# Optimization experiments

Measured on AMD Instinct MI355X. Metric: run time of the kernel, lower is better.

The kernel has to match this reference:

```python
import jax, jax.numpy as jnp
import numpy as np

# --- static config (from init_kwargs) ---
DT, TAU_M = 1.0, 10.0
BETA = float(np.exp(-DT / TAU_M))
THRESH = 1.0
SLOPE = 25.0  # fast_sigmoid surrogate slope
T, B, DEPTH, SZ = 50, 16, 1, 64
C1, C2, K1, K2 = 16, 16, 5, 5
S1 = SZ - K1 + 1   # 60
S2 = S1 - K2 + 1   # 56
NCONV2 = C2 * S2 * S2  # 50176
NREC = 256

@jax.custom_vjp
def spike(m):
    return (m > THRESH).astype(m.dtype)

def _spk_fwd(m):
    return spike(m), m

def _spk_bwd(m, g):
    # fast_sigmoid surrogate: d spk / d mem = 1 / (slope*|mem - thr| + 1)^2
    return (g / (SLOPE * jnp.abs(m - THRESH) + 1.0) ** 2,)

spike.defvjp(_spk_fwd, _spk_bwd)

def lif(inp, mem, zero_reset=False):
    # snntorch Leaky: reset computed from previous mem, detached
    reset = jax.lax.stop_gradient((mem > THRESH).astype(mem.dtype))
    base = BETA * mem + inp
    mem_new = base * (1.0 - reset) if zero_reset else base - reset * THRESH
    return spike(mem_new), mem_new

def conv(x, w, b):
    y = jax.lax.conv_general_dilated(x, w, (1, 1), 'VALID',
                                     dimension_numbers=('NCHW', 'OIHW', 'NCHW'))
    return y + b[None, :, None, None]

def deconv(x, w, b):
    # torch ConvTranspose2d (stride 1, no pad), weight [Cin, Cout, kh, kw]
    k = w.shape[-1]
    wf = jnp.flip(w, (2, 3)).transpose(1, 0, 2, 3)  # -> OIHW, O=Cout
    y = jax.lax.conv_general_dilated(x, wf, (1, 1),
                                     [(k - 1, k - 1), (k - 1, k - 1)],
                                     dimension_numbers=('NCHW', 'OIHW', 'NCHW'))
    return y + b[None, :, None, None]

def setup_inputs() -> dict:
    key = jax.random.key(0)
    ks = jax.random.split(key, 16)
    def w(k, shape, fan_in):
        return (jax.random.normal(k, shape, jnp.float32) / np.sqrt(fan_in)).astype(jnp.float32)
    # osc_of_t per process_params: R_m*I_osc/v_th*(1-beta)*(-1+cos(omega*t - pi))/2
    tarr = np.arange(0, T * DT, DT)
    omega = 2 * np.pi * 0.01
    osc = (1.0 * 1.0 / 1.0) * (1 - BETA) * (-1 + np.cos(omega * tarr - np.pi)) / 2
    return {
        'x': jax.random.normal(ks[0], (T, B, DEPTH, SZ, SZ), jnp.float32),
        'osc': jnp.asarray(osc, jnp.float32),
        'conv1_w': w(ks[1], (C1, DEPTH, K1, K1), DEPTH * K1 * K1),
        'conv1_b': jnp.zeros((C1,), jnp.float32),
        'conv2_w': w(ks[2], (C2, C1, K2, K2), C1 * K2 * K2),
        'conv2_b': jnp.zeros((C2,), jnp.float32),
        'ff_in_w': w(ks[3], (NREC, NCONV2), NCONV2),
        'ff_in_b': jnp.zeros((NREC,), jnp.float32),
        'ff_rec_w': w(ks[4], (NREC, NREC), NREC),
        'ff_rec_b': jnp.zeros((NREC,), jnp.float32),
        'ff_out_w': w(ks[5], (NCONV2, NREC), NREC),
        'ff_out_b': jnp.zeros((NCONV2,), jnp.float32),
        'deconv2_w': w(ks[6], (C2, C1, K2, K2), C2 * K2 * K2),
        'deconv2_b': jnp.zeros((C1,), jnp.float32),
        'recon_w': w(ks[7], (C1, DEPTH, K1, K1), C1 * K1 * K1),
        'recon_b': jnp.zeros((DEPTH,), jnp.float32),
    }

def reference(x, osc, conv1_w, conv1_b, conv2_w, conv2_b,
              ff_in_w, ff_in_b, ff_rec_w, ff_rec_b, ff_out_w, ff_out_b,
              deconv2_w, deconv2_b, recon_w, recon_b):
    mem_c1 = jnp.zeros((B, C1, S1, S1), x.dtype)
    mem_c2 = jnp.zeros((B, C2, S2, S2), x.dtype)
    mem_rec = jnp.zeros((B, NREC), x.dtype)
    mem_d2 = jnp.zeros((B, C1, S1, S1), x.dtype)
    mem_rc = jnp.zeros((B, DEPTH, SZ, SZ), x.dtype)
    spk_rec0 = jnp.zeros((B, NREC), x.dtype)

    def step(carry, xt_osc):
        mem_c1, mem_c2, mem_rec, mem_d2, mem_rc, spk_rec = carry
        xt, o = xt_osc
        spk1, mem_c1 = lif(conv(xt, conv1_w, conv1_b) + o, mem_c1)
        spk2, mem_c2 = lif(conv(spk1, conv2_w, conv2_b) + o, mem_c2)
        curr_in = spk2.reshape(B, -1) @ ff_in_w.T + ff_in_b
        curr_rec = spk_rec @ ff_rec_w.T + ff_rec_b
        spk_rec, mem_rec = lif(curr_in + curr_rec + o, mem_rec, zero_reset=True)
        curr_out = (spk_rec @ ff_out_w.T + ff_out_b).reshape(B, C2, S2, S2)
        spk_d2, mem_d2 = lif(deconv(curr_out, deconv2_w, deconv2_b) + o, mem_d2)
        spk_rc, mem_rc = lif(deconv(spk_d2, recon_w, recon_b) + o, mem_rc)
        return (mem_c1, mem_c2, mem_rec, mem_d2, mem_rc, spk_rec), (spk_rec, spk_rc)

    carry0 = (mem_c1, mem_c2, mem_rec, mem_d2, mem_rc, spk_rec0)
    _, (spk_recs, spk_outs) = jax.lax.scan(step, carry0, (x, osc))
    return spk_recs, spk_outs
```

## Files before the change

kernel.cpp:

```cpp
#include <hip/hip_runtime.h>

#define BETA_F 0.9048374180359595f

constexpr int B_ = 16, C1_ = 16, C2_ = 16;
constexpr int S1 = 60, S2 = 56;
constexpr int NCONV2 = C2_ * S2 * S2;
constexpr int NREC = 256;

__device__ float g_mem_c1x[2 * 921600];
__device__ float g_mem_c2[802816];
__device__ float g_mem_rec[4096];
__device__ float g_mem_d2[921600];
__device__ float g_mem_rc[65536];
__device__ unsigned char g_spk2bx[2][B_ * NCONV2];
__device__ float g_currx[2][B_ * NCONV2];
__device__ float g_spkd2x[2][921600];
__device__ float g_spkrec2[2 * 4096];
__device__ float g_woutT[NREC * NCONV2];

__device__ __forceinline__ float lif_sub(float mp, float inp, float& mn_out) {
    float rst = mp > 1.f ? 1.f : 0.f;
    float base = __fadd_rn(__fmul_rn(BETA_F, mp), inp);
    float mn = __fsub_rn(base, rst);
    mn_out = mn;
    return mn > 1.f ? 1.f : 0.f;
}

__global__ void k_transpose(const float* __restrict__ Wout) {
    __shared__ float T[64][65];
    int m0 = blockIdx.x * 64;
    for (int k0 = 0; k0 < 256; k0 += 64) {
        __syncthreads();
        for (int e = threadIdx.x; e < 64 * 64; e += 256) {
            int i = e >> 6, k = e & 63;
            T[i][k] = Wout[(size_t)(m0 + i) * 256 + k0 + k];
        }
        __syncthreads();
        for (int e = threadIdx.x; e < 64 * 64; e += 256) {
            int k = e >> 6, i = e & 63;
            g_woutT[(size_t)(k0 + k) * NCONV2 + m0 + i] = T[i][k];
        }
    }
}

__global__ __launch_bounds__(256)
void k_wave(int kw,
            const float* __restrict__ x, const float* __restrict__ osc,
            const float* __restrict__ w1, const float* __restrict__ b1,
            const float* __restrict__ w2, const float* __restrict__ b2,
            const float* __restrict__ win, const float* __restrict__ bin,
            const float* __restrict__ wrec, const float* __restrict__ brec,
            const float* __restrict__ bout,
            const float* __restrict__ wd2, const float* __restrict__ bd2,
            const float* __restrict__ wrc, const float* __restrict__ brc,
            float* __restrict__ out_recs, float* __restrict__ out_outs) {
    __shared__ float smem[8704];
    const int r = blockIdx.x;
    const int tid = threadIdx.x;

    if (r < 448) {
        int t = kw;
        if (t > 49) return;
        int first = (t == 0) ? 1 : 0;
        float* xw = smem;
        float* s1 = smem + 768;
        int tile = r % 14, b = (r / 14) & 15, half = r / 224;
        int y0 = 4 * tile;
        int y1 = (tile == 13) ? 60 : (y0 + 4);
        const float* xin = x + ((size_t)t * B_ + b) * 4096;
        for (int e = tid; e < 12 * 64; e += 256)
            xw[e] = xin[(y0 + (e >> 6)) * 64 + (e & 63)];
        __syncthreads();

        int par = t & 1;
        float* mc1_new = g_mem_c1x + (size_t)par * 921600;
        const float* mc1_old = g_mem_c1x + (size_t)(1 - par) * 921600;
        unsigned char* spk2b = g_spk2bx[par];
        float osct = osc[t];
#pragma unroll 1
        for (int c = 0; c < 16; c++) {
            const float* wc = w1 + c * 25;
            float bc = b1[c];
            for (int e = tid; e < 8 * 60; e += 256) {
                int rr = e / 60, col = e % 60;
                float s = 0.f;
#pragma unroll
                for (int ky = 0; ky < 5; ky++)
#pragma unroll
                    for (int kx = 0; kx < 5; kx++)
                        s = fmaf(xw[(rr + ky) * 64 + col + kx], wc[ky * 5 + kx], s);
                float inp = __fadd_rn(__fadd_rn(s, bc), osct);
                int gr = y0 + rr;
                int gidx = ((b * 16 + c) * 60 + gr) * 60 + col;
                float mp = first ? 0.f : mc1_old[gidx];
                float mn;
                float spk = lif_sub(mp, inp, mn);
                if (half == 0 && gr >= y0 && gr < y1) mc1_new[gidx] = mn;
                s1[c * 480 + e] = spk;
            }
        }
        __syncthreads();

        if (tid >= 224) return;
        int p = tile * 224 + tid;
        int yy = p / 56, xx = p % 56;
        int c2lo = half * 8;
        float acc[8];
#pragma unroll
        for (int u = 0; u < 8; u++) acc[u] = 0.f;
#pragma unroll 1
        for (int ci = 0; ci < 16; ci++) {
            const float* ip = s1 + ci * 480 + (yy - y0) * 60 + xx;
            float ipv[25];
#pragma unroll
            for (int ky = 0; ky < 5; ky++)
#pragma unroll
                for (int kx = 0; kx < 5; kx++)
                    ipv[ky * 5 + kx] = ip[ky * 60 + kx];
#pragma unroll
            for (int u = 0; u < 8; u++) {
                const float* wp = w2 + (c2lo + u) * 400 + ci * 25;
                float s = acc[u];
#pragma unroll
                for (int k = 0; k < 25; k++)
                    s = fmaf(ipv[k], wp[k], s);
                acc[u] = s;
            }
        }
#pragma unroll 1
        for (int u = 0; u < 8; u++) {
            int c2 = c2lo + u;
            float inp = __fadd_rn(__fadd_rn(acc[u], b2[c2]), osct);
            int idx = (b * 16 + c2) * 3136 + p;
            float mp = first ? 0.f : g_mem_c2[idx];
            float mn;
            float spk = lif_sub(mp, inp, mn);
            g_mem_c2[idx] = mn;
            spk2b[idx] = (unsigned char)(spk > 0.5f ? 1 : 0);
        }
    } else if (r < 1472) {
        int t = kw - 1;
        if (t < 0 || t > 49) return;
        int first = (t == 0) ? 1 : 0;
        float* red = smem;
        float* sprev = smem + 256;
        float* cur = smem + 1280;
        int bid = r - 448;
        int n = ((bid >> 5) << 3) + (bid & 7);
        int bg = ((bid >> 3) & 3) * 4;
        int par = t & 1;
        const float* sp_old = g_spkrec2 + (size_t)(1 - par) * 4096;
#pragma unroll
        for (int l = 0; l < 4; l++) {
            int e = tid + l * 256;
            sprev[e] = first ? 0.f : sp_old[(bg + (e >> 8)) * 256 + (e & 255)];
        }
        const unsigned char* sbase = g_spk2bx[par];
        const float* wrow = win + (size_t)n * NCONV2;
        const unsigned char* s0 = sbase + (size_t)(bg + 0) * NCONV2;
        const unsigned char* s1p = sbase + (size_t)(bg + 1) * NCONV2;
        const unsigned char* s2 = sbase + (size_t)(bg + 2) * NCONV2;
        const unsigned char* s3 = sbase + (size_t)(bg + 3) * NCONV2;
        float a0 = 0.f, a1 = 0.f, a2 = 0.f, a3 = 0.f;
        for (int j = 0; j < 49; j++) {
            int k = tid + j * 1024;
            float w0 = wrow[k];
            float wA = wrow[k + 256];
            float wB = wrow[k + 512];
            float wC = wrow[k + 768];
            unsigned char p00 = s0[k],       p01 = s1p[k],       p02 = s2[k],       p03 = s3[k];
            unsigned char p10 = s0[k + 256], p11 = s1p[k + 256], p12 = s2[k + 256], p13 = s3[k + 256];
            unsigned char p20 = s0[k + 512], p21 = s1p[k + 512], p22 = s2[k + 512], p23 = s3[k + 512];
            unsigned char p30 = s0[k + 768], p31 = s1p[k + 768], p32 = s2[k + 768], p33 = s3[k + 768];
            a0 = fmaf((float)p00, w0, a0); a1 = fmaf((float)p01, w0, a1);
            a2 = fmaf((float)p02, w0, a2); a3 = fmaf((float)p03, w0, a3);
            a0 = fmaf((float)p10, wA, a0); a1 = fmaf((float)p11, wA, a1);
            a2 = fmaf((float)p12, wA, a2); a3 = fmaf((float)p13, wA, a3);
            a0 = fmaf((float)p20, wB, a0); a1 = fmaf((float)p21, wB, a1);
            a2 = fmaf((float)p22, wB, a2); a3 = fmaf((float)p23, wB, a3);
            a0 = fmaf((float)p30, wC, a0); a1 = fmaf((float)p31, wC, a1);
            a2 = fmaf((float)p32, wC, a2); a3 = fmaf((float)p33, wC, a3);
        }
        float accs[4] = {a0, a1, a2, a3};
#pragma unroll
        for (int u = 0; u < 4; u++) {
            red[tid] = accs[u];
            __syncthreads();
            for (int st = 128; st > 0; st >>= 1) {
                if (tid < st) red[tid] = __fadd_rn(red[tid], red[tid + st]);
                __syncthreads();
            }
            if (tid == 0) cur[u] = red[0];
            __syncthreads();
        }
        if (tid < 4) {
            int bb = bg + tid;
            const float* wr = wrec + (size_t)n * 256;
            float acc = 0.f;
            for (int k = 0; k < 256; k++) acc = fmaf(sprev[tid * 256 + k], wr[k], acc);
            float cin = __fadd_rn(cur[tid], bin[n]);
            float crc = __fadd_rn(acc, brec[n]);
            float inp = __fadd_rn(__fadd_rn(cin, crc), osc[t]);
            int idx = bb * 256 + n;
            float mp = first ? 0.f : g_mem_rec[idx];
            float rst = mp > 1.f ? 1.f : 0.f;
            float base = __fadd_rn(__fmul_rn(BETA_F, mp), inp);
            float mn = (rst > 0.f) ? 0.f : base;
            g_mem_rec[idx] = mn;
            float spk = mn > 1.f ? 1.f : 0.f;
            g_spkrec2[(size_t)par * 4096 + idx] = spk;
            out_recs[(size_t)t * 4096 + idx] = spk;
        }
    } else if (r < 1864) {
        int t = kw - 2;
        if (t < 0 || t > 49) return;
        float* S = smem;
        int r2 = r - 1472;
        int mblk = r2 % 196;
        int bhalf = (r2 / 196) * 8;
        int par = t & 1;
#pragma unroll
        for (int l = 0; l < 8; l++) {
            int e = tid + l * 256;
            S[(e >> 8) * 256 + (e & 255)] =
                g_spkrec2[(size_t)par * 4096 + (bhalf + (e >> 8)) * 256 + (e & 255)];
        }
        __syncthreads();
        int m = mblk * 256 + tid;
        float* currw = g_currx[par];
        float acc[8];
#pragma unroll
        for (int b = 0; b < 8; b++) acc[b] = 0.f;
        for (int k = 0; k < 256; k++) {
            float w = g_woutT[(size_t)k * NCONV2 + m];
#pragma unroll
            for (int b = 0; b < 8; b++) acc[b] = fmaf(S[b * 256 + k], w, acc[b]);
        }
        float bb = bout[m];
#pragma unroll
        for (int b = 0; b < 8; b++)
            currw[(size_t)(bhalf + b) * NCONV2 + m] = __fadd_rn(acc[b], bb);
    } else if (r < 2344) {
        int t = kw - 3;
        if (t < 0 || t > 49) return;
        int first = (t == 0) ? 1 : 0;
        float* sd = smem;
        int r3 = r - 1864;
        int tile = r3 % 15, b = (r3 / 15) & 15, half = r3 / 240;
        int r0 = 4 * tile;
        int y0p = r0 - 4;
        int par = t & 1;
        const float* in = g_currx[par] + (size_t)b * NCONV2;
        for (int e = tid; e < 16 * 8 * 64; e += 256) {
            int ci = e / 512;
            int rem = e - ci * 512;
            int rr = rem >> 6, j = rem & 63;
            int iy = y0p + rr;
            int ix = j - 4;
            float v = (iy >= 0 && iy < 56 && ix >= 0 && ix < 56)
                        ? in[ci * 3136 + iy * 56 + ix] : 0.f;
            sd[e] = v;
        }
        __syncthreads();
        if (tid >= 240) return;
        int p = r0 * 60 + tid;
        int yy = p / 60, xx = p % 60;
        int colo = half * 8;
        float acc[8];
#pragma unroll
        for (int u = 0; u < 8; u++) acc[u] = 0.f;
#pragma unroll
        for (int kp = 0; kp < 5; kp++) {
            int rr = yy - r0 + kp;
#pragma unroll 1
            for (int ci = 0; ci < 16; ci++) {
                const float* ip = sd + ci * 512 + rr * 64 + xx;
                float ipv[5];
#pragma unroll
                for (int kq = 0; kq < 5; kq++) ipv[kq] = ip[kq];
#pragma unroll
                for (int u = 0; u < 8; u++) {
                    const float* wp = wd2 + (ci * 16 + colo + u) * 25 + (4 - kp) * 5;
                    float s = acc[u];
#pragma unroll
                    for (int kq = 0; kq < 5; kq++)
                        s = fmaf(ipv[kq], wp[4 - kq], s);
                    acc[u] = s;
                }
            }
        }
        float osct = osc[t];
        float* spkd2w = g_spkd2x[par];
#pragma unroll 1
        for (int u = 0; u < 8; u++) {
            int co = colo + u;
            float inp = __fadd_rn(__fadd_rn(acc[u], bd2[co]), osct);
            int idx = (b * 16 + co) * 3600 + p;
            float mp = first ? 0.f : g_mem_d2[idx];
            float mn;
            float spk = lif_sub(mp, inp, mn);
            g_mem_d2[idx] = mn;
            spkd2w[idx] = spk;
        }
    } else {
        int t = kw - 4;
        if (t < 0 || t > 49) return;
        int first = (t == 0) ? 1 : 0;
        float* sd = smem;
        int r4 = r - 2344;
        int tile = r4 & 15, b = r4 >> 4;
        int yymin = tile * 4;
        int y0p = yymin - 4;
        int par = t & 1;
        const float* in = g_spkd2x[par] + (size_t)b * 16 * 3600;
        for (int e = tid; e < 16 * 8 * 68; e += 256) {
            int ci = e / 544;
            int rem = e - ci * 544;
            int rr = rem / 68, j = rem - rr * 68;
            int iy = y0p + rr;
            int ix = j - 4;
            float v = (iy >= 0 && iy < 60 && ix >= 0 && ix < 60)
                        ? in[ci * 3600 + iy * 60 + ix] : 0.f;
            sd[e] = v;
        }
        __syncthreads();
        int p = tile * 256 + tid;
        int yy = p >> 6, xx = p & 63;
        float s = 0.f;
#pragma unroll
        for (int kp = 0; kp < 5; kp++) {
            int rr = yy - yymin + kp;
#pragma unroll 1
            for (int ci = 0; ci < 16; ci++) {
                const float* ip = sd + ci * 544 + rr * 68 + xx;
                const float* wp = wrc + ci * 25 + (4 - kp) * 5;
#pragma unroll
                for (int kq = 0; kq < 5; kq++)
                    s = fmaf(ip[kq], wp[4 - kq], s);
            }
        }
        float inp = __fadd_rn(__fadd_rn(s, brc[0]), osc[t]);
        int idx = b * 4096 + p;
        float mp = first ? 0.f : g_mem_rc[idx];
        float mn;
        float spk = lif_sub(mp, inp, mn);
        g_mem_rc[idx] = mn;
        out_outs[(size_t)t * B_ * 4096 + idx] = spk;
    }
}

extern "C" void kernel_launch(void* const* d_in, const int* in_sizes, int n_in,
                              void* d_out, int out_size, void* d_ws, size_t ws_size,
                              hipStream_t stream) {
    const float* x    = (const float*)d_in[0];
    const float* osc  = (const float*)d_in[1];
    const float* w1   = (const float*)d_in[2];
    const float* b1   = (const float*)d_in[3];
    const float* w2   = (const float*)d_in[4];
    const float* b2   = (const float*)d_in[5];
    const float* win  = (const float*)d_in[6];
    const float* bin  = (const float*)d_in[7];
    const float* wrec = (const float*)d_in[8];
    const float* brec = (const float*)d_in[9];
    const float* wout = (const float*)d_in[10];
    const float* bout = (const float*)d_in[11];
    const float* wd2  = (const float*)d_in[12];
    const float* bd2  = (const float*)d_in[13];
    const float* wrc  = (const float*)d_in[14];
    const float* brc  = (const float*)d_in[15];

    float* out = (float*)d_out;
    float* out_recs = out;
    float* out_outs = out + 50 * 16 * 256;

    k_transpose<<<784, 256, 0, stream>>>(wout);
    for (int kw = 0; kw < 54; kw++) {
        k_wave<<<2600, 256, 0, stream>>>(kw, x, osc, w1, b1, w2, b2, win, bin,
                                         wrec, brec, bout, wd2, bd2, wrc, brc,
                                         out_recs, out_outs);
    }
}
```

Baseline: 5.531 ms.

## Interleave conv2 spikes by batch, unroll ff_in loop, split recon tiles finer

Stores conv2 spike bytes batch-interleaved (16 batches per position) so the ff_in stage loads four batches with one uchar4 load instead of four scattered byte loads, and unrolls that loop twice. Conv1 now reads the input directly from global memory instead of staging it in shared memory, which drops one barrier. The recon stage is split into twice as many smaller tiles using 128 threads each, and the grid grows to match; the ff_out loop gets unroll 4. The interleaved layout makes conv2's byte stores strided, and half the threads in each recon block sit idle.

```diff
diff --git a/kernel.cpp b/kernel.cpp
--- a/kernel.cpp
+++ b/kernel.cpp
@@ -12,7 +12,7 @@
 __device__ float g_mem_rec[4096];
 __device__ float g_mem_d2[921600];
 __device__ float g_mem_rc[65536];
-__device__ unsigned char g_spk2bx[2][B_ * NCONV2];
+__device__ unsigned char g_spkpx[2][NCONV2 * 16];
 __device__ float g_currx[2][B_ * NCONV2];
 __device__ float g_spkd2x[2][921600];
 __device__ float g_spkrec2[2 * 4096];
@@ -54,7 +54,7 @@
             const float* __restrict__ wd2, const float* __restrict__ bd2,
             const float* __restrict__ wrc, const float* __restrict__ brc,
             float* __restrict__ out_recs, float* __restrict__ out_outs) {
-    __shared__ float smem[8704];
+    __shared__ float smem[8192];
     const int r = blockIdx.x;
     const int tid = threadIdx.x;
 
@@ -62,20 +62,16 @@
         int t = kw;
         if (t > 49) return;
         int first = (t == 0) ? 1 : 0;
-        float* xw = smem;
-        float* s1 = smem + 768;
+        float* s1 = smem;
         int tile = r % 14, b = (r / 14) & 15, half = r / 224;
         int y0 = 4 * tile;
         int y1 = (tile == 13) ? 60 : (y0 + 4);
         const float* xin = x + ((size_t)t * B_ + b) * 4096;
-        for (int e = tid; e < 12 * 64; e += 256)
-            xw[e] = xin[(y0 + (e >> 6)) * 64 + (e & 63)];
-        __syncthreads();
 
         int par = t & 1;
         float* mc1_new = g_mem_c1x + (size_t)par * 921600;
         const float* mc1_old = g_mem_c1x + (size_t)(1 - par) * 921600;
-        unsigned char* spk2b = g_spk2bx[par];
+        unsigned char* spkp = g_spkpx[par];
         float osct = osc[t];
 #pragma unroll 1
         for (int c = 0; c < 16; c++) {
@@ -88,14 +84,14 @@
                 for (int ky = 0; ky < 5; ky++)
 #pragma unroll
                     for (int kx = 0; kx < 5; kx++)
-                        s = fmaf(xw[(rr + ky) * 64 + col + kx], wc[ky * 5 + kx], s);
+                        s = fmaf(xin[(y0 + rr + ky) * 64 + col + kx], wc[ky * 5 + kx], s);
                 float inp = __fadd_rn(__fadd_rn(s, bc), osct);
                 int gr = y0 + rr;
                 int gidx = ((b * 16 + c) * 60 + gr) * 60 + col;
                 float mp = first ? 0.f : mc1_old[gidx];
                 float mn;
                 float spk = lif_sub(mp, inp, mn);
-                if (half == 0 && gr >= y0 && gr < y1) mc1_new[gidx] = mn;
+                if (half == 0 && gr < y1) mc1_new[gidx] = mn;
                 s1[c * 480 + e] = spk;
             }
         }
@@ -136,7 +132,7 @@
             float mn;
             float spk = lif_sub(mp, inp, mn);
             g_mem_c2[idx] = mn;
-            spk2b[idx] = (unsigned char)(spk > 0.5f ? 1 : 0);
+            spkp[(size_t)(c2 * 3136 + p) * 16 + b] = (unsigned char)(spk > 0.5f ? 1 : 0);
         }
     } else if (r < 1472) {
         int t = kw - 1;
@@ -155,31 +151,64 @@
             int e = tid + l * 256;
             sprev[e] = first ? 0.f : sp_old[(bg + (e >> 8)) * 256 + (e & 255)];
         }
-        const unsigned char* sbase = g_spk2bx[par];
+        const unsigned char* spb = g_spkpx[par] + bg;
         const float* wrow = win + (size_t)n * NCONV2;
-        const unsigned char* s0 = sbase + (size_t)(bg + 0) * NCONV2;
-        const unsigned char* s1p = sbase + (size_t)(bg + 1) * NCONV2;
-        const unsigned char* s2 = sbase + (size_t)(bg + 2) * NCONV2;
-        const unsigned char* s3 = sbase + (size_t)(bg + 3) * NCONV2;
         float a0 = 0.f, a1 = 0.f, a2 = 0.f, a3 = 0.f;
-        for (int j = 0; j < 49; j++) {
-            int k = tid + j * 1024;
+#pragma unroll 1
+        for (int jj = 0; jj < 24; jj++) {
+            int k = tid + (2 * jj) * 1024;
+            int k2 = k + 1024;
             float w0 = wrow[k];
             float wA = wrow[k + 256];
             float wB = wrow[k + 512];
             float wC = wrow[k + 768];
-            unsigned char p00 = s0[k],       p01 = s1p[k],       p02 = s2[k],       p03 = s3[k];
-            unsigned char p10 = s0[k + 256], p11 = s1p[k + 256], p12 = s2[k + 256], p13 = s3[k + 256];
-            unsigned char p20 = s0[k + 512], p21 = s1p[k + 512], p22 = s2[k + 512], p23 = s3[k + 512];
-            unsigned char p30 = s0[k + 768], p31 = s1p[k + 768], p32 = s2[k + 768], p33 = s3[k + 768];
-            a0 = fmaf((float)p00, w0, a0); a1 = fmaf((float)p01, w0, a1);
-            a2 = fmaf((float)p02, w0, a2); a3 = fmaf((float)p03, w0, a3);
-            a0 = fmaf((float)p10, wA, a0); a1 = fmaf((float)p11, wA, a1);
-            a2 = fmaf((float)p12, wA, a2); a3 = fmaf((float)p13, wA, a3);
-            a0 = fmaf((float)p20, wB, a0); a1 = fmaf((float)p21, wB, a1);
-            a2 = fmaf((float)p22, wB, a2); a3 = fmaf((float)p23, wB, a3);
-            a0 = fmaf((float)p30, wC, a0); a1 = fmaf((float)p31, wC, a1);
-            a2 = fmaf((float)p32, wC, a2); a3 = fmaf((float)p33, wC, a3);
+            float v0 = wrow[k2];
+            float vA = wrow[k2 + 256];
+            float vB = wrow[k2 + 512];
+            float vC = wrow[k2 + 768];
+            uchar4 q0 = *reinterpret_cast<const uchar4*>(spb + (size_t)k * 16);
+            uchar4 q1 = *reinterpret_cast<const uchar4*>(spb + (size_t)(k + 256) * 16);
+            uchar4 q2 = *reinterpret_cast<const uchar4*>(spb + (size_t)(k + 512) * 16);
+            uchar4 q3 = *reinterpret_cast<const uchar4*>(spb + (size_t)(k + 768) * 16);
+            uchar4 r0 = *reinterpret_cast<const uchar4*>(spb + (size_t)k2 * 16);
+            uchar4 r1 = *reinterpret_cast<const uchar4*>(spb + (size_t)(k2 + 256) * 16);
+            uchar4 r2 = *reinterpret_cast<const uchar4*>(spb + (size_t)(k2 + 512) * 16);
+            uchar4 r3 = *reinterpret_cast<const uchar4*>(spb + (size_t)(k2 + 768) * 16);
+            a0 = fmaf((float)q0.x, w0, a0); a1 = fmaf((float)q0.y, w0, a1);
+            a2 = fmaf((float)q0.z, w0, a2); a3 = fmaf((float)q0.w, w0, a3);
+            a0 = fmaf((float)q1.x, wA, a0); a1 = fmaf((float)q1.y, wA, a1);
+            a2 = fmaf((float)q1.z, wA, a2); a3 = fmaf((float)q1.w, wA, a3);
+            a0 = fmaf((float)q2.x, wB, a0); a1 = fmaf((float)q2.y, wB, a1);
+            a2 = fmaf((float)q2.z, wB, a2); a3 = fmaf((float)q2.w, wB, a3);
+            a0 = fmaf((float)q3.x, wC, a0); a1 = fmaf((float)q3.y, wC, a1);
+            a2 = fmaf((float)q3.z, wC, a2); a3 = fmaf((float)q3.w, wC, a3);
+            a0 = fmaf((float)r0.x, v0, a0); a1 = fmaf((float)r0.y, v0, a1);
+            a2 = fmaf((float)r0.z, v0, a2); a3 = fmaf((float)r0.w, v0, a3);
+            a0 = fmaf((float)r1.x, vA, a0); a1 = fmaf((float)r1.y, vA, a1);
+            a2 = fmaf((float)r1.z, vA, a2); a3 = fmaf((float)r1.w, vA, a3);
+            a0 = fmaf((float)r2.x, vB, a0); a1 = fmaf((float)r2.y, vB, a1);
+            a2 = fmaf((float)r2.z, vB, a2); a3 = fmaf((float)r2.w, vB, a3);
+            a0 = fmaf((float)r3.x, vC, a0); a1 = fmaf((float)r3.y, vC, a1);
+            a2 = fmaf((float)r3.z, vC, a2); a3 = fmaf((float)r3.w, vC, a3);
+        }
+        {
+            int k = tid + 48 * 1024;
+            float w0 = wrow[k];
+            float wA = wrow[k + 256];
+            float wB = wrow[k + 512];
+            float wC = wrow[k + 768];
+            uchar4 q0 = *reinterpret_cast<const uchar4*>(spb + (size_t)k * 16);
+            uchar4 q1 = *reinterpret_cast<const uchar4*>(spb + (size_t)(k + 256) * 16);
+            uchar4 q2 = *reinterpret_cast<const uchar4*>(spb + (size_t)(k + 512) * 16);
+            uchar4 q3 = *reinterpret_cast<const uchar4*>(spb + (size_t)(k + 768) * 16);
+            a0 = fmaf((float)q0.x, w0, a0); a1 = fmaf((float)q0.y, w0, a1);
+            a2 = fmaf((float)q0.z, w0, a2); a3 = fmaf((float)q0.w, w0, a3);
+            a0 = fmaf((float)q1.x, wA, a0); a1 = fmaf((float)q1.y, wA, a1);
+            a2 = fmaf((float)q1.z, wA, a2); a3 = fmaf((float)q1.w, wA, a3);
+            a0 = fmaf((float)q2.x, wB, a0); a1 = fmaf((float)q2.y, wB, a1);
+            a2 = fmaf((float)q2.z, wB, a2); a3 = fmaf((float)q2.w, wB, a3);
+            a0 = fmaf((float)q3.x, wC, a0); a1 = fmaf((float)q3.y, wC, a1);
+            a2 = fmaf((float)q3.z, wC, a2); a3 = fmaf((float)q3.w, wC, a3);
         }
         float accs[4] = {a0, a1, a2, a3};
 #pragma unroll
@@ -231,6 +260,7 @@
         float acc[8];
 #pragma unroll
         for (int b = 0; b < 8; b++) acc[b] = 0.f;
+#pragma unroll 4
         for (int k = 0; k < 256; k++) {
             float w = g_woutT[(size_t)k * NCONV2 + m];
 #pragma unroll
@@ -308,14 +338,14 @@
         int first = (t == 0) ? 1 : 0;
         float* sd = smem;
         int r4 = r - 2344;
-        int tile = r4 & 15, b = r4 >> 4;
-        int yymin = tile * 4;
+        int tile = r4 & 31, b = r4 >> 5;
+        int yymin = tile * 2;
         int y0p = yymin - 4;
         int par = t & 1;
         const float* in = g_spkd2x[par] + (size_t)b * 16 * 3600;
-        for (int e = tid; e < 16 * 8 * 68; e += 256) {
-            int ci = e / 544;
-            int rem = e - ci * 544;
+        for (int e = tid; e < 16 * 6 * 68; e += 256) {
+            int ci = e / 408;
+            int rem = e - ci * 408;
             int rr = rem / 68, j = rem - rr * 68;
             int iy = y0p + rr;
             int ix = j - 4;
@@ -324,7 +354,8 @@
             sd[e] = v;
         }
         __syncthreads();
-        int p = tile * 256 + tid;
+        if (tid >= 128) return;
+        int p = yymin * 64 + tid;
         int yy = p >> 6, xx = p & 63;
         float s = 0.f;
 #pragma unroll
@@ -332,7 +363,7 @@
             int rr = yy - yymin + kp;
 #pragma unroll 1
             for (int ci = 0; ci < 16; ci++) {
-                const float* ip = sd + ci * 544 + rr * 68 + xx;
+                const float* ip = sd + ci * 408 + rr * 68 + xx;
                 const float* wp = wrc + ci * 25 + (4 - kp) * 5;
 #pragma unroll
                 for (int kq = 0; kq < 5; kq++)
@@ -375,7 +406,7 @@
 
     k_transpose<<<784, 256, 0, stream>>>(wout);
     for (int kw = 0; kw < 54; kw++) {
-        k_wave<<<2600, 256, 0, stream>>>(kw, x, osc, w1, b1, w2, b2, win, bin,
+        k_wave<<<2856, 256, 0, stream>>>(kw, x, osc, w1, b1, w2, b2, win, bin,
                                          wrec, brec, bout, wd2, bd2, wrc, brc,
                                          out_recs, out_outs);
     }
```

New measurement: 6.002 ms. +8.5%, slower.
